# Performance work log

Measured on AMD Instinct MI355X. Metric: run time of the kernel, lower is better.

The kernel has to match this reference:

```python
import jax, jax.numpy as jnp
import numpy as np

NEG_SLOPE = 0.01  # PyTorch LeakyReLU default


def leaky(x):
    return jnp.where(x >= 0, x, NEG_SLOPE * x)


def conv(x, w, b, stride, pad):
    # x: NCHW, w: OIHW
    y = jax.lax.conv_general_dilated(
        x, w, (stride, stride), [(pad, pad), (pad, pad)],
        dimension_numbers=("NCHW", "OIHW", "NCHW"))
    return y + b[None, :, None, None]


def conv_transpose(x, w, b, stride, pad):
    # w has PyTorch ConvTranspose2d layout (in, out, kh, kw)
    wf = jnp.flip(w, (2, 3)).transpose(1, 0, 2, 3)  # -> (out, in, kh, kw)
    k = w.shape[2]
    p = k - 1 - pad
    y = jax.lax.conv_general_dilated(
        x, wf, (1, 1), [(p, p), (p, p)], lhs_dilation=(stride, stride),
        dimension_numbers=("NCHW", "OIHW", "NCHW"))
    return y + b[None, :, None, None]


def setup_inputs() -> dict:
    key = jax.random.key(0)
    ks = jax.random.split(key, 16)
    D, K = 64, 512
    s = 0.05
    inp = {
        "x": jax.random.normal(ks[0], (64, 1, 128, 128), jnp.float32),
        # encoder
        "ew1": jax.random.normal(ks[1], (8, 1, 4, 4), jnp.float32) * s,
        "eb1": jnp.zeros((8,), jnp.float32),
        "ew2": jax.random.normal(ks[2], (16, 8, 4, 4), jnp.float32) * s,
        "eb2": jnp.zeros((16,), jnp.float32),
        "ew3": jax.random.normal(ks[3], (16, 16, 3, 3), jnp.float32) * s,
        "eb3": jnp.zeros((16,), jnp.float32),
        "ew4": jax.random.normal(ks[4], (D, 16, 1, 1), jnp.float32) * s,
        "eb4": jnp.zeros((D,), jnp.float32),
        # codebook, init uniform(-1/K, 1/K) as in the module
        "codebook": jax.random.uniform(ks[5], (K, D), jnp.float32, -1.0 / K, 1.0 / K),
        # decoder
        "dw1": jax.random.normal(ks[6], (16, D, 3, 3), jnp.float32) * s,
        "db1": jnp.zeros((16,), jnp.float32),
        "dw2": jax.random.normal(ks[7], (16, 8, 4, 4), jnp.float32) * s,  # ConvT (in,out,k,k)
        "db2": jnp.zeros((8,), jnp.float32),
        "dw3": jax.random.normal(ks[8], (8, 1, 4, 4), jnp.float32) * s,  # ConvT (in,out,k,k)
        "db3": jnp.zeros((1,), jnp.float32),
    }
    return inp


BETA = 0.25


def vq(latents_nchw, codebook):
    # latents -> NHWC
    lat = jnp.transpose(latents_nchw, (0, 2, 3, 1))
    shp = lat.shape
    D = shp[-1]
    flat = lat.reshape(-1, D)  # [M, D]
    # pairwise squared distances to codebook [M, K]
    dist = (jnp.sum(flat ** 2, axis=1, keepdims=True)
            + jnp.sum(codebook ** 2, axis=1)
            - 2.0 * flat @ codebook.T)
    inds = jnp.argmin(dist, axis=1)  # [M]
    quant = codebook[inds].reshape(shp)  # gather == one-hot @ codebook
    commitment_loss = jnp.mean((jax.lax.stop_gradient(quant) - lat) ** 2)
    embedding_loss = jnp.mean((quant - jax.lax.stop_gradient(lat)) ** 2)
    vq_loss = commitment_loss * BETA + embedding_loss
    # straight-through estimator
    quant = lat + jax.lax.stop_gradient(quant - lat)
    return jnp.transpose(quant, (0, 3, 1, 2)), vq_loss


def reference(x, ew1, eb1, ew2, eb2, ew3, eb3, ew4, eb4, codebook,
              dw1, db1, dw2, db2, dw3, db3):
    # encoder
    h = leaky(conv(x, ew1, eb1, 2, 1))
    h = leaky(conv(h, ew2, eb2, 2, 1))
    h = leaky(conv(h, ew3, eb3, 1, 1))
    h = leaky(conv(h, ew4, eb4, 1, 0))
    # vector quantization
    q, vq_loss = vq(h, codebook)
    # decoder
    d = leaky(conv(q, dw1, db1, 1, 1))
    d = leaky(conv_transpose(d, dw2, db2, 2, 1))
    d = jnp.tanh(conv_transpose(d, dw3, db3, 2, 1))
    return d, vq_loss
```

## Files before the change

kernel.cpp:

```cpp
#include <hip/hip_runtime.h>
#include <math.h>

#define DEV __device__ __forceinline__
DEV float leakyf(float v) { return v >= 0.f ? v : 0.01f * v; }
DEV int rfl(int v) { return __builtin_amdgcn_readfirstlane(v); }

struct F4 { float x, y, z, w; };

#define OFF_XP   0u
#define OFF_H1P  1081600u
#define OFF_H2P  3311872u
#define OFF_H3   4495616u
#define OFF_D1P  5544192u
#define OFF_D2P  6727936u
#define OFF_IDX  8958208u
#define OFF_U    9023744u
#define OFF_C2   9097472u
#define OFF_W4T  9097984u
#define OFF_DWT  9099008u
#define OFF_LOSS 9108224u

DEV void halo_store(float* base, int plane, int r, int W, int H, long psz)
{
    int row, col;
    if (r < W)          { row = 0;     col = r; }
    else if (r < 2 * W) { row = H - 1; col = r - W; }
    else { int r2 = r - 2 * W; row = 1 + (r2 >> 1); col = (r2 & 1) ? W - 1 : 0; }
    base[plane * psz + row * W + col] = 0.f;
}

__global__ void setup_k(const float* __restrict__ x, const float* __restrict__ ew4,
                        const float* __restrict__ dw1, const float* __restrict__ cb,
                        float* __restrict__ ws)
{
    int id = blockIdx.x * 256 + threadIdx.x;
    {
        int ix = id & 127, iy = (id >> 7) & 127, n = id >> 14;
        ws[OFF_XP + (n * 130 + iy + 1) * 130 + ix + 1] = x[id];
    }
    if (id < 33024) {
        halo_store(ws + OFF_XP, id / 516, id % 516, 130, 130, 16900);
    } else if (id < 166144) {
        int i = id - 33024;
        halo_store(ws + OFF_H1P, i / 260, i % 260, 66, 66, 4356);
    } else if (id < 301312) {
        int i = id - 166144;
        halo_store(ws + OFF_H2P, i / 132, i % 132, 34, 34, 1156);
    } else if (id < 436480) {
        int i = id - 301312;
        halo_store(ws + OFF_D1P, i / 132, i % 132, 34, 34, 1156);
    } else if (id < 569600) {
        int i = id - 436480;
        halo_store(ws + OFF_D2P, i / 260, i % 260, 66, 66, 4356);
    }
    if (id < 1024) {
        int d = id & 63, ci = id >> 6;
        ws[OFF_W4T + id] = ew4[d * 16 + ci];
    } else if (id < 1536) {
        int k = id - 1024;
        float s = 0.f;
        #pragma unroll
        for (int d = 0; d < 64; ++d) { float v = cb[k * 64 + d]; s = fmaf(v, v, s); }
        ws[OFF_C2 + k] = s;
    } else if (id == 1536) {
        ws[OFF_LOSS] = 0.f;
    } else if (id >= 2048 && id < 11264) {
        int i = id - 2048;
        int co = i & 15, tap = (i >> 4) % 9, ci = i / 144;
        ws[OFF_DWT + i] = dw1[(co * 64 + ci) * 9 + tap];
    }
}

__global__ void uprep_k(const float* __restrict__ dwT, const float* __restrict__ cb,
                        float* __restrict__ U)
{
    int id = blockIdx.x * 256 + threadIdx.x;
    int k = id / 144;
    int r = id - k * 144;
    float s = 0.f;
    #pragma unroll
    for (int ci = 0; ci < 64; ++ci)
        s = fmaf(cb[k * 64 + ci], dwT[ci * 144 + r], s);
    U[id] = s;
}

__global__ __launch_bounds__(256) void e1p_k(const float* __restrict__ xp,
                                             const float* __restrict__ ew1,
                                             const float* __restrict__ eb1,
                                             float* __restrict__ h1p)
{
    __shared__ float wl[128];
    int t = threadIdx.x;
    if (t < 128) { int co = t & 7, tap = t >> 3; wl[t] = ew1[co * 16 + tap]; }
    __syncthreads();
    int id = blockIdx.x * 256 + t;
    int x = id & 63, y = (id >> 6) & 63, n = id >> 12;
    float acc[8];
    #pragma unroll
    for (int j = 0; j < 8; ++j) acc[j] = eb1[j];
    const float* base = xp + (n * 130 + 2 * y) * 130 + 2 * x;
    #pragma unroll
    for (int ky = 0; ky < 4; ++ky) {
        F4 v = *(const F4*)(base + ky * 130);
        float vv[4] = { v.x, v.y, v.z, v.w };
        #pragma unroll
        for (int kx = 0; kx < 4; ++kx) {
            const float* wp = &wl[(ky * 4 + kx) * 8];
            #pragma unroll
            for (int j = 0; j < 8; ++j) acc[j] = fmaf(vv[kx], wp[j], acc[j]);
        }
    }
    #pragma unroll
    for (int j = 0; j < 8; ++j)
        h1p[((n * 8 + j) * 66 + y + 1) * 66 + x + 1] = leakyf(acc[j]);
}

__global__ __launch_bounds__(256) void e2p_k(const float* __restrict__ h1p,
                                             const float* __restrict__ ew2,
                                             const float* __restrict__ eb2,
                                             float* __restrict__ h2p)
{
    __shared__ float wl[512];
    int t = threadIdx.x;
    int id = blockIdx.x * 256 + t;
    int x = id & 31, y = (id >> 5) & 31;
    int cg = rfl((id >> 10) & 3), n = id >> 12;
    for (int i = t; i < 512; i += 256) {
        int co = i & 3, r = i >> 2;
        int kx = r & 3, ky = (r >> 2) & 3, ci = r >> 4;
        wl[i] = ew2[((cg * 4 + co) * 8 + ci) * 16 + ky * 4 + kx];
    }
    __syncthreads();
    float acc[4];
    #pragma unroll
    for (int j = 0; j < 4; ++j) acc[j] = eb2[cg * 4 + j];
    #pragma unroll 1
    for (int ci = 0; ci < 8; ++ci) {
        const float* base = h1p + ((n * 8 + ci) * 66 + 2 * y) * 66 + 2 * x;
        #pragma unroll
        for (int ky = 0; ky < 4; ++ky) {
            F4 v = *(const F4*)(base + ky * 66);
            float vv[4] = { v.x, v.y, v.z, v.w };
            #pragma unroll
            for (int kx = 0; kx < 4; ++kx) {
                const float* wp = &wl[((ci * 4 + ky) * 4 + kx) * 4];
                acc[0] = fmaf(vv[kx], wp[0], acc[0]);
                acc[1] = fmaf(vv[kx], wp[1], acc[1]);
                acc[2] = fmaf(vv[kx], wp[2], acc[2]);
                acc[3] = fmaf(vv[kx], wp[3], acc[3]);
            }
        }
    }
    #pragma unroll
    for (int j = 0; j < 4; ++j)
        h2p[((n * 16 + cg * 4 + j) * 34 + y + 1) * 34 + x + 1] = leakyf(acc[j]);
}

__global__ __launch_bounds__(256) void e3p_k(const float* __restrict__ h2p,
                                             const float* __restrict__ ew3,
                                             const float* __restrict__ eb3,
                                             float* __restrict__ h3)
{
    __shared__ float wl[576];
    int t = threadIdx.x;
    int id = blockIdx.x * 256 + t;
    int x = id & 31, y = (id >> 5) & 31;
    int cg = rfl((id >> 10) & 3), n = id >> 12;
    for (int i = t; i < 576; i += 256) {
        int co = i & 3, r = i >> 2;
        int kx = r % 3, ky = (r / 3) % 3, ci = r / 9;
        wl[i] = ew3[((cg * 4 + co) * 16 + ci) * 9 + ky * 3 + kx];
    }
    __syncthreads();
    float acc[4];
    #pragma unroll
    for (int j = 0; j < 4; ++j) acc[j] = eb3[cg * 4 + j];
    #pragma unroll 1
    for (int ci = 0; ci < 16; ++ci) {
        const float* base = h2p + ((n * 16 + ci) * 34 + y) * 34 + x;
        #pragma unroll
        for (int ky = 0; ky < 3; ++ky) {
            F4 v = *(const F4*)(base + ky * 34);
            float vv[3] = { v.x, v.y, v.z };
            #pragma unroll
            for (int kx = 0; kx < 3; ++kx) {
                const float* wp = &wl[((ci * 3 + ky) * 3 + kx) * 4];
                acc[0] = fmaf(vv[kx], wp[0], acc[0]);
                acc[1] = fmaf(vv[kx], wp[1], acc[1]);
                acc[2] = fmaf(vv[kx], wp[2], acc[2]);
                acc[3] = fmaf(vv[kx], wp[3], acc[3]);
            }
        }
    }
    #pragma unroll
    for (int j = 0; j < 4; ++j)
        h3[((n * 16 + cg * 4 + j) << 10) + (y << 5) + x] = leakyf(acc[j]);
}

__global__ __launch_bounds__(256) void vqh_k(const float* __restrict__ h3,
                                             const float* __restrict__ w4t,
                                             const float* __restrict__ eb4,
                                             const float* __restrict__ cb,
                                             const float* __restrict__ c2,
                                             int* __restrict__ idxOut,
                                             float* __restrict__ lossAcc)
{
    __shared__ float Fs[64 * 128];
    __shared__ float Cs[64 * 128];
    int t = threadIdx.x;
    int row0 = blockIdx.x << 7;
    int n = row0 >> 10;
    int pos0 = row0 & 1023;

    {
        int row = t & 127, dh = t >> 7;
        const float* hp = h3 + (n << 14) + pos0 + row;
        float h[16];
        #pragma unroll
        for (int ci = 0; ci < 16; ++ci) h[ci] = hp[ci << 10];
        #pragma unroll
        for (int q = 0; q < 8; ++q) {
            int d0 = dh * 32 + q * 4;
            float a0 = eb4[d0 + 0], a1 = eb4[d0 + 1];
            float a2 = eb4[d0 + 2], a3 = eb4[d0 + 3];
            #pragma unroll
            for (int ci = 0; ci < 16; ++ci) {
                float v = h[ci];
                const float* wp = w4t + (ci << 6) + d0;
                a0 = fmaf(v, wp[0], a0); a1 = fmaf(v, wp[1], a1);
                a2 = fmaf(v, wp[2], a2); a3 = fmaf(v, wp[3], a3);
            }
            Fs[(d0 + 0) * 128 + row] = leakyf(a0);
            Fs[(d0 + 1) * 128 + row] = leakyf(a1);
            Fs[(d0 + 2) * 128 + row] = leakyf(a2);
            Fs[(d0 + 3) * 128 + row] = leakyf(a3);
        }
    }

    int tr = t & 15, tc = t >> 4;
    float best[8]; int bk[8];
    #pragma unroll
    for (int i = 0; i < 8; ++i) { best[i] = 3.4e38f; bk[i] = 0; }

    #pragma unroll 1
    for (int p = 0; p < 4; ++p) {
        __syncthreads();
        {
            int code = t >> 1, dh = t & 1;
            const float* src = cb + (((p << 7) + code) << 6) + dh * 32;
            #pragma unroll
            for (int q = 0; q < 8; ++q) {
                float4 v = *(const float4*)(src + q * 4);
                int d0 = dh * 32 + q * 4;
                Cs[(d0 + 0) * 128 + code] = v.x;
                Cs[(d0 + 1) * 128 + code] = v.y;
                Cs[(d0 + 2) * 128 + code] = v.z;
                Cs[(d0 + 3) * 128 + code] = v.w;
            }
        }
        __syncthreads();

        float acc[8][8];
        #pragma unroll
        for (int i = 0; i < 8; ++i)
            #pragma unroll
            for (int j = 0; j < 8; ++j) acc[i][j] = 0.f;

        const float* fp0 = &Fs[tr * 4];
        const float* fp1 = &Fs[64 + tr * 4];
        const float* cp0 = &Cs[tc * 4];
        const float* cp1 = &Cs[64 + tc * 4];
        #pragma unroll 8
        for (int d = 0; d < 64; ++d) {
            float4 f0 = *(const float4*)(fp0 + d * 128);
            float4 f1 = *(const float4*)(fp1 + d * 128);
            float4 c0 = *(const float4*)(cp0 + d * 128);
            float4 c1 = *(const float4*)(cp1 + d * 128);
            float f[8] = { f0.x, f0.y, f0.z, f0.w, f1.x, f1.y, f1.z, f1.w };
            float c[8] = { c0.x, c0.y, c0.z, c0.w, c1.x, c1.y, c1.z, c1.w };
            #pragma unroll
            for (int i = 0; i < 8; ++i)
                #pragma unroll
                for (int j = 0; j < 8; ++j)
                    acc[i][j] = fmaf(f[i], c[j], acc[i][j]);
        }
        #pragma unroll
        for (int j = 0; j < 8; ++j) {
            int kk = (p << 7) + (j < 4 ? tc * 4 + j : 64 + tc * 4 + j - 4);
            float hc2 = 0.5f * c2[kk];
            #pragma unroll
            for (int i = 0; i < 8; ++i) {
                float s = hc2 - acc[i][j];
                if (s < best[i]) { best[i] = s; bk[i] = kk; }
            }
        }
    }

    __syncthreads();
    float* redS = Cs;
    int*   redI = (int*)(Cs + 2176);
    #pragma unroll
    for (int i = 0; i < 8; ++i) {
        int row = (i < 4) ? tr * 4 + i : 64 + tr * 4 + i - 4;
        redS[row * 17 + tc] = best[i];
        redI[row * 17 + tc] = bk[i];
    }
    __syncthreads();
    if (t < 128) {
        int row = t;
        float bs = redS[row * 17]; int bi = redI[row * 17];
        #pragma unroll
        for (int c = 1; c < 16; ++c) {
            float s2 = redS[row * 17 + c];
            int   i2 = redI[row * 17 + c];
            if (s2 < bs || (s2 == bs && i2 < bi)) { bs = s2; bi = i2; }
        }
        idxOut[row0 + row] = bi;
        const float* cr = cb + (bi << 6);
        float rs = 0.f;
        #pragma unroll
        for (int d = 0; d < 64; ++d) {
            float e = cr[d] - Fs[d * 128 + row];
            rs = fmaf(e, e, rs);
        }
        #pragma unroll
        for (int off = 32; off; off >>= 1) rs += __shfl_down(rs, off, 64);
        if ((t & 63) == 0) atomicAdd(lossAcc, rs);
    }
}

__global__ __launch_bounds__(256) void d1p_k(const int* __restrict__ idx,
                                             const float* __restrict__ U,
                                             const float* __restrict__ db1,
                                             const float* __restrict__ lossAcc,
                                             float* __restrict__ lossOut,
                                             float* __restrict__ d1p)
{
    int id = blockIdx.x * 256 + threadIdx.x;
    if (id == 0) lossOut[0] = 1.25f * lossAcc[0] / 4194304.0f;
    int x = id & 31, y = (id >> 5) & 31;
    int cg = rfl((id >> 10) & 3), n = id >> 12;
    float acc[4];
    #pragma unroll
    for (int j = 0; j < 4; ++j) acc[j] = db1[cg * 4 + j];
    const float4* U4 = (const float4*)U;
    #pragma unroll
    for (int tap = 0; tap < 9; ++tap) {
        int yy = y + tap / 3 - 1, xx = x + tap % 3 - 1;
        if (yy < 0 || yy > 31 || xx < 0 || xx > 31) continue;
        int k = idx[(n << 10) + (yy << 5) + xx];
        float4 u = U4[(k * 9 + tap) * 4 + cg];
        acc[0] += u.x; acc[1] += u.y; acc[2] += u.z; acc[3] += u.w;
    }
    #pragma unroll
    for (int j = 0; j < 4; ++j)
        d1p[((n * 16 + cg * 4 + j) * 34 + y + 1) * 34 + x + 1] = leakyf(acc[j]);
}

__global__ __launch_bounds__(256) void dt2p_k(const float* __restrict__ d1p,
                                              const float* __restrict__ dw2,
                                              const float* __restrict__ db2,
                                              float* __restrict__ d2p)
{
    __shared__ float wl[512];
    int t = threadIdx.x;
    int id = blockIdx.x * 256 + t;
    int x = id & 31, y = (id >> 5) & 31;
    int cg = rfl((id >> 10) & 3), n = id >> 12;
    for (int i = t; i < 512; i += 256) {
        int co = i & 1, tap = (i >> 1) & 15, ci = i >> 5;
        wl[i] = dw2[(ci * 8 + cg * 2 + co) * 16 + tap];
    }
    __syncthreads();
    float acc[2][2][2];
    #pragma unroll
    for (int py = 0; py < 2; ++py)
        #pragma unroll
        for (int px = 0; px < 2; ++px)
            #pragma unroll
            for (int j = 0; j < 2; ++j) acc[py][px][j] = db2[cg * 2 + j];
    #pragma unroll 1
    for (int ci = 0; ci < 16; ++ci) {
        const float* base = d1p + ((n * 16 + ci) * 34 + y) * 34 + x;
        F4 r0 = *(const F4*)(base);
        F4 r1 = *(const F4*)(base + 34);
        F4 r2 = *(const F4*)(base + 68);
        float v[3][3] = { { r0.x, r0.y, r0.z },
                          { r1.x, r1.y, r1.z },
                          { r2.x, r2.y, r2.z } };
        #pragma unroll
        for (int ky = 0; ky < 4; ++ky) {
            int py = (ky + 1) & 1;
            int dy = (ky == 0) ? 1 : (ky == 3 ? -1 : 0);
            #pragma unroll
            for (int kx = 0; kx < 4; ++kx) {
                int px = (kx + 1) & 1;
                int dx = (kx == 0) ? 1 : (kx == 3 ? -1 : 0);
                float vv = v[dy + 1][dx + 1];
                const float* wp = &wl[(ci * 16 + ky * 4 + kx) * 2];
                acc[py][px][0] = fmaf(vv, wp[0], acc[py][px][0]);
                acc[py][px][1] = fmaf(vv, wp[1], acc[py][px][1]);
            }
        }
    }
    #pragma unroll
    for (int py = 0; py < 2; ++py)
        #pragma unroll
        for (int px = 0; px < 2; ++px)
            #pragma unroll
            for (int j = 0; j < 2; ++j)
                d2p[((n * 8 + cg * 2 + j) * 66 + 2 * y + py + 1) * 66 + 2 * x + px + 1] =
                    leakyf(acc[py][px][j]);
}

__global__ __launch_bounds__(256) void dt3p_k(const float* __restrict__ d2p,
                                              const float* __restrict__ dw3,
                                              const float* __restrict__ db3,
                                              float* __restrict__ out)
{
    int id = blockIdx.x * 256 + threadIdx.x;
    int x = id & 63, y = (id >> 6) & 63, n = id >> 12;
    float b = db3[0];
    float acc[2][2] = { { b, b }, { b, b } };
    #pragma unroll 1
    for (int ci = 0; ci < 8; ++ci) {
        const float* base = d2p + ((n * 8 + ci) * 66 + y) * 66 + x;
        F4 r0 = *(const F4*)(base);
        F4 r1 = *(const F4*)(base + 66);
        F4 r2 = *(const F4*)(base + 132);
        float v[3][3] = { { r0.x, r0.y, r0.z },
                          { r1.x, r1.y, r1.z },
                          { r2.x, r2.y, r2.z } };
        #pragma unroll
        for (int ky = 0; ky < 4; ++ky) {
            int py = (ky + 1) & 1;
            int dy = (ky == 0) ? 1 : (ky == 3 ? -1 : 0);
            #pragma unroll
            for (int kx = 0; kx < 4; ++kx) {
                int px = (kx + 1) & 1;
                int dx = (kx == 0) ? 1 : (kx == 3 ? -1 : 0);
                acc[py][px] = fmaf(v[dy + 1][dx + 1], dw3[ci * 16 + ky * 4 + kx],
                                   acc[py][px]);
            }
        }
    }
    #pragma unroll
    for (int py = 0; py < 2; ++py)
        #pragma unroll
        for (int px = 0; px < 2; ++px)
            out[(n << 14) + ((2 * y + py) << 7) + 2 * x + px] = tanhf(acc[py][px]);
}

extern "C" void kernel_launch(void* const* d_in, const int* in_sizes, int n_in,
                              void* d_out, int out_size, void* d_ws, size_t ws_size,
                              hipStream_t stream)
{
    const float* x        = (const float*)d_in[0];
    const float* ew1      = (const float*)d_in[1];
    const float* eb1      = (const float*)d_in[2];
    const float* ew2      = (const float*)d_in[3];
    const float* eb2      = (const float*)d_in[4];
    const float* ew3      = (const float*)d_in[5];
    const float* eb3      = (const float*)d_in[6];
    const float* ew4      = (const float*)d_in[7];
    const float* eb4      = (const float*)d_in[8];
    const float* codebook = (const float*)d_in[9];
    const float* dw1      = (const float*)d_in[10];
    const float* db1      = (const float*)d_in[11];
    const float* dw2      = (const float*)d_in[12];
    const float* db2      = (const float*)d_in[13];
    const float* dw3      = (const float*)d_in[14];
    const float* db3      = (const float*)d_in[15];

    float* out = (float*)d_out;
    float* ws  = (float*)d_ws;
    float* XP   = ws + OFF_XP;
    float* H1P  = ws + OFF_H1P;
    float* H2P  = ws + OFF_H2P;
    float* H3   = ws + OFF_H3;
    float* D1P  = ws + OFF_D1P;
    float* D2P  = ws + OFF_D2P;
    int*   IDX  = (int*)(ws + OFF_IDX);
    float* U    = ws + OFF_U;
    float* C2   = ws + OFF_C2;
    float* W4T  = ws + OFF_W4T;
    float* DWT  = ws + OFF_DWT;
    float* LOSS = ws + OFF_LOSS;

    setup_k<<<4096, 256, 0, stream>>>(x, ew4, dw1, codebook, ws);
    uprep_k<<<288, 256, 0, stream>>>(DWT, codebook, U);

    e1p_k<<<1024, 256, 0, stream>>>(XP, ew1, eb1, H1P);
    e2p_k<<<1024, 256, 0, stream>>>(H1P, ew2, eb2, H2P);
    e3p_k<<<1024, 256, 0, stream>>>(H2P, ew3, eb3, H3);

    vqh_k<<<512, 256, 0, stream>>>(H3, W4T, eb4, codebook, C2, IDX, LOSS);

    d1p_k<<<1024, 256, 0, stream>>>(IDX, U, db1, LOSS, out + 1048576, D1P);
    dt2p_k<<<1024, 256, 0, stream>>>(D1P, dw2, db2, D2P);
    dt3p_k<<<1024, 256, 0, stream>>>(D2P, dw3, db3, out);
}
```

Before: 134.0 us.

## Pre-transpose codebook, fold U precompute into setup, derive VQ loss from distance

New measurement: 158.4 us. +18.3%, slower.

```diff
diff --git a/kernel.cpp b/kernel.cpp
--- a/kernel.cpp
+++ b/kernel.cpp
@@ -17,8 +17,8 @@
 #define OFF_U    9023744u
 #define OFF_C2   9097472u
 #define OFF_W4T  9097984u
-#define OFF_DWT  9099008u
-#define OFF_LOSS 9108224u
+#define OFF_LOSS 9099008u
+#define OFF_CT   9099264u
 
 DEV void halo_store(float* base, int plane, int r, int W, int H, long psz)
 {
@@ -64,24 +64,20 @@
         ws[OFF_C2 + k] = s;
     } else if (id == 1536) {
         ws[OFF_LOSS] = 0.f;
-    } else if (id >= 2048 && id < 11264) {
-        int i = id - 2048;
-        int co = i & 15, tap = (i >> 4) % 9, ci = i / 144;
-        ws[OFF_DWT + i] = dw1[(co * 64 + ci) * 9 + tap];
-    }
-}
-
-__global__ void uprep_k(const float* __restrict__ dwT, const float* __restrict__ cb,
-                        float* __restrict__ U)
-{
-    int id = blockIdx.x * 256 + threadIdx.x;
-    int k = id / 144;
-    int r = id - k * 144;
-    float s = 0.f;
-    #pragma unroll
-    for (int ci = 0; ci < 64; ++ci)
-        s = fmaf(cb[k * 64 + ci], dwT[ci * 144 + r], s);
-    U[id] = s;
+    } else if (id >= 16384 && id < 49152) {
+        int i = id - 16384;
+        ws[OFF_CT + i] = cb[((i & 511) << 6) + (i >> 9)];
+    } else if (id >= 131072 && id < 204800) {
+        int i = id - 131072;
+        int k = i / 144;
+        int r = i - k * 144;
+        int tap = r >> 4, co = r & 15;
+        float s = 0.f;
+        #pragma unroll
+        for (int ci = 0; ci < 64; ++ci)
+            s = fmaf(cb[k * 64 + ci], dw1[(co * 64 + ci) * 9 + tap], s);
+        ws[OFF_U + i] = s;
+    }
 }
 
 __global__ __launch_bounds__(256) void e1p_k(const float* __restrict__ xp,
@@ -197,16 +193,17 @@
         h3[((n * 16 + cg * 4 + j) << 10) + (y << 5) + x] = leakyf(acc[j]);
 }
 
-__global__ __launch_bounds__(256) void vqh_k(const float* __restrict__ h3,
+__global__ __launch_bounds__(256) void vqm_k(const float* __restrict__ h3,
                                              const float* __restrict__ w4t,
                                              const float* __restrict__ eb4,
-                                             const float* __restrict__ cb,
+                                             const float* __restrict__ ct,
                                              const float* __restrict__ c2,
                                              int* __restrict__ idxOut,
                                              float* __restrict__ lossAcc)
 {
     __shared__ float Fs[64 * 128];
     __shared__ float Cs[64 * 128];
+    __shared__ float f2s[256];
     int t = threadIdx.x;
     int row0 = blockIdx.x << 7;
     int n = row0 >> 10;
@@ -218,6 +215,7 @@
         float h[16];
         #pragma unroll
         for (int ci = 0; ci < 16; ++ci) h[ci] = hp[ci << 10];
+        float f2 = 0.f;
         #pragma unroll
         for (int q = 0; q < 8; ++q) {
             int d0 = dh * 32 + q * 4;
@@ -230,11 +228,16 @@
                 a0 = fmaf(v, wp[0], a0); a1 = fmaf(v, wp[1], a1);
                 a2 = fmaf(v, wp[2], a2); a3 = fmaf(v, wp[3], a3);
             }
-            Fs[(d0 + 0) * 128 + row] = leakyf(a0);
-            Fs[(d0 + 1) * 128 + row] = leakyf(a1);
-            Fs[(d0 + 2) * 128 + row] = leakyf(a2);
-            Fs[(d0 + 3) * 128 + row] = leakyf(a3);
-        }
+            float l0 = leakyf(a0), l1 = leakyf(a1);
+            float l2 = leakyf(a2), l3 = leakyf(a3);
+            Fs[(d0 + 0) * 128 + row] = l0;
+            Fs[(d0 + 1) * 128 + row] = l1;
+            Fs[(d0 + 2) * 128 + row] = l2;
+            Fs[(d0 + 3) * 128 + row] = l3;
+            f2 = fmaf(l0, l0, f2); f2 = fmaf(l1, l1, f2);
+            f2 = fmaf(l2, l2, f2); f2 = fmaf(l3, l3, f2);
+        }
+        f2s[dh * 128 + row] = f2;
     }
 
     int tr = t & 15, tc = t >> 4;
@@ -246,16 +249,11 @@
     for (int p = 0; p < 4; ++p) {
         __syncthreads();
         {
-            int code = t >> 1, dh = t & 1;
-            const float* src = cb + (((p << 7) + code) << 6) + dh * 32;
+            int d0 = t >> 5, c0 = (t & 31) << 2;
             #pragma unroll
             for (int q = 0; q < 8; ++q) {
-                float4 v = *(const float4*)(src + q * 4);
-                int d0 = dh * 32 + q * 4;
-                Cs[(d0 + 0) * 128 + code] = v.x;
-                Cs[(d0 + 1) * 128 + code] = v.y;
-                Cs[(d0 + 2) * 128 + code] = v.z;
-                Cs[(d0 + 3) * 128 + code] = v.w;
+                float4 v = *(const float4*)(ct + ((q * 8 + d0) << 9) + (p << 7) + c0);
+                *(float4*)&Cs[q * 1024 + t * 4] = v;
             }
         }
         __syncthreads();
@@ -316,13 +314,7 @@
             if (s2 < bs || (s2 == bs && i2 < bi)) { bs = s2; bi = i2; }
         }
         idxOut[row0 + row] = bi;
-        const float* cr = cb + (bi << 6);
-        float rs = 0.f;
-        #pragma unroll
-        for (int d = 0; d < 64; ++d) {
-            float e = cr[d] - Fs[d * 128 + row];
-            rs = fmaf(e, e, rs);
-        }
+        float rs = 2.f * bs + f2s[row] + f2s[128 + row];
         #pragma unroll
         for (int off = 32; off; off >>= 1) rs += __shfl_down(rs, off, 64);
         if ((t & 63) == 0) atomicAdd(lossAcc, rs);
@@ -484,17 +476,16 @@
     float* U    = ws + OFF_U;
     float* C2   = ws + OFF_C2;
     float* W4T  = ws + OFF_W4T;
-    float* DWT  = ws + OFF_DWT;
     float* LOSS = ws + OFF_LOSS;
+    float* CT   = ws + OFF_CT;
 
     setup_k<<<4096, 256, 0, stream>>>(x, ew4, dw1, codebook, ws);
-    uprep_k<<<288, 256, 0, stream>>>(DWT, codebook, U);
 
     e1p_k<<<1024, 256, 0, stream>>>(XP, ew1, eb1, H1P);
     e2p_k<<<1024, 256, 0, stream>>>(H1P, ew2, eb2, H2P);
     e3p_k<<<1024, 256, 0, stream>>>(H2P, ew3, eb3, H3);
 
-    vqh_k<<<512, 256, 0, stream>>>(H3, W4T, eb4, codebook, C2, IDX, LOSS);
+    vqm_k<<<512, 256, 0, stream>>>(H3, W4T, eb4, CT, C2, IDX, LOSS);
 
     d1p_k<<<1024, 256, 0, stream>>>(IDX, U, db1, LOSS, out + 1048576, D1P);
     dt2p_k<<<1024, 256, 0, stream>>>(D1P, dw2, db2, D2P);
```
